# Kernel tuning notes

Hardware: AMD Instinct MI355X
Metric: run time of the kernel (lower is better)

Reference implementation:

```python
import jax, jax.numpy as jnp
import numpy as np

N_NODES = 64
KS = (52, 42, 34)  # ceil(0.8*64), ceil(0.8*52), ceil(0.8*42)


def _gcn(x, A, W, b):
    # GCNConv(improved=True): self-loop fill 2.0, symmetric normalization. A[tgt, src], weighted.
    n = A.shape[0]
    Ah = A + 2.0 * jnp.eye(n, dtype=A.dtype)
    d = Ah.sum(-1)
    dis = jnp.where(d > 0, jax.lax.rsqrt(d), 0.0)
    An = dis[:, None] * Ah * dis[None, :]
    return An @ (x @ W) + b


def _augment(A):
    # GraphUNet.augment_adj: add self loops (weight 1), A2 = A1 @ A1, remove self loops
    n = A.shape[0]
    eye = jnp.eye(n, dtype=A.dtype)
    A1 = A + eye
    return (A1 @ A1) * (1.0 - eye)


def _pool(x, A, w, k):
    # TopKPooling: score = tanh(x.w/||w||), keep top-k, scale kept features by score
    s = jnp.tanh((x @ w) / jnp.linalg.norm(w))
    sv, perm = jax.lax.top_k(s, k)
    return x[perm] * sv[:, None], A[perm][:, perm], perm


def _unet(x, A, dw0, db0, dws, dbs, pws, uws, ubs, uwl, ubl):
    # GraphUNet(depth=3, sum_res=True), single graph: x [n, F2], A [n, n]
    x = jax.nn.relu(_gcn(x, A, dw0, db0))
    xs, As, perms = [x], [A], []
    for i in range(3):
        A = _augment(A)
        x, A, perm = _pool(x, A, pws[i], KS[i])
        x = jax.nn.relu(_gcn(x, A, dws[i], dbs[i]))
        if i < 2:
            xs.append(x)
            As.append(A)
        perms.append(perm)
    for i in range(3):
        j = 2 - i
        res, Aj, perm = xs[j], As[j], perms[j]
        x = res + jnp.zeros_like(res).at[perm].set(x)
        if i < 2:
            x = jax.nn.relu(_gcn(x, Aj, uws[i], ubs[i]))
        else:
            x = _gcn(x, Aj, uwl, ubl)
    return x


def _nnconv(x, src, dst, ea, mw, mb, rw, bias):
    # NNConv(aggr='mean'): per-edge MLP weight, gather-matmul-scatter-mean + root + bias
    B, E = src.shape
    fin, fout = rw.shape
    We = jax.nn.relu(ea @ mw + mb).reshape(B, E, fin, fout)  # [B,E,fin,fout]
    xs = jnp.take_along_axis(x, src[..., None], axis=1)      # [B,E,fin]
    msg = jnp.einsum('bei,beio->beo', xs, We)                # [B,E,fout]
    seg = jax.vmap(lambda m, d: jax.ops.segment_sum(m, d, num_segments=N_NODES))
    sums = seg(msg, dst)
    cnt = seg(jnp.ones(msg.shape[:2] + (1,), msg.dtype), dst)
    agg = sums / jnp.maximum(cnt, 1.0)
    return agg + x @ rw + bias


def _adj(src, dst):
    A = jnp.zeros((N_NODES, N_NODES), jnp.float32).at[dst, src].set(1.0)
    return A * (1.0 - jnp.eye(N_NODES, dtype=jnp.float32))


def _branch(x, ei, ea, mlp1, mlp2, u1, u2):
    src, dst = ei[:, 0], ei[:, 1]
    A = jax.vmap(_adj)(src, dst)
    x = jax.nn.relu(_nnconv(x, src, dst, ea, *mlp1))
    x = jax.nn.relu(jax.vmap(lambda h, a: _unet(h, a, *u1))(x, A))
    x = jax.nn.relu(_nnconv(x, src, dst, ea, *mlp2))
    x = jax.nn.relu(jax.vmap(lambda h, a: _unet(h, a, *u2))(x, A))
    return x.mean(axis=1)  # global_mean_pool (equal-sized graphs)


def setup_inputs() -> dict:
    key = jax.random.key(0)
    keys = iter(jax.random.split(key, 64))
    def nrm(shape, s=1.0):
        return jax.random.normal(next(keys), shape, jnp.float32) * s
    B, n, E, F, F2, Q, H, C = 128, 64, 512, 64, 32, 16, 256, 50
    inp = {}
    inp['x1'] = nrm((B, n, F))
    inp['ei1'] = jax.random.randint(next(keys), (B, 2, E), 0, n, jnp.int32)
    inp['ea1'] = jax.random.uniform(next(keys), (B, E, 1), jnp.float32)
    inp['jw1'] = nrm((B, Q))
    inp['x2'] = nrm((B, n, F))
    inp['ei2'] = jax.random.randint(next(keys), (B, 2, E), 0, n, jnp.int32)
    inp['ea2'] = jax.random.uniform(next(keys), (B, E, 1), jnp.float32)
    inp['jw2'] = nrm((B, Q))
    inp['m1w'] = nrm((1, F * F2), 0.1)
    inp['m1b'] = nrm((F * F2,), 0.1)
    inp['r1w'] = nrm((F, F2), 0.1)
    inp['c1b'] = nrm((F2,), 0.1)
    inp['m2w'] = nrm((1, F2 * F2), 0.1)
    inp['m2b'] = nrm((F2 * F2,), 0.1)
    inp['r2w'] = nrm((F2, F2), 0.1)
    inp['c2b'] = nrm((F2,), 0.1)
    for p in ('u1', 'u2'):
        inp[p + '_dw0'] = nrm((F2, C), 0.1)
        inp[p + '_db0'] = nrm((C,), 0.1)
        inp[p + '_dws'] = nrm((3, C, C), 0.1)
        inp[p + '_dbs'] = nrm((3, C), 0.1)
        inp[p + '_pws'] = nrm((3, C), 0.1)
        inp[p + '_uws'] = nrm((2, C, C), 0.1)
        inp[p + '_ubs'] = nrm((2, C), 0.1)
        inp[p + '_uwl'] = nrm((C, F2), 0.1)
        inp[p + '_ubl'] = nrm((F2,), 0.1)
    inp['bb_w'] = nrm(((F2 + Q) * 2, H), 0.1)
    inp['bb_b'] = nrm((H,), 0.1)
    return inp


def reference(x1, ei1, ea1, jw1, x2, ei2, ea2, jw2,
              m1w, m1b, r1w, c1b, m2w, m2b, r2w, c2b,
              u1_dw0, u1_db0, u1_dws, u1_dbs, u1_pws, u1_uws, u1_ubs, u1_uwl, u1_ubl,
              u2_dw0, u2_db0, u2_dws, u2_dbs, u2_pws, u2_uws, u2_ubs, u2_uwl, u2_ubl,
              bb_w, bb_b):
    mlp1 = (m1w, m1b, r1w, c1b)
    mlp2 = (m2w, m2b, r2w, c2b)
    u1 = (u1_dw0, u1_db0, u1_dws, u1_dbs, u1_pws, u1_uws, u1_ubs, u1_uwl, u1_ubl)
    u2 = (u2_dw0, u2_db0, u2_dws, u2_dbs, u2_pws, u2_uws, u2_ubs, u2_uwl, u2_ubl)
    r1 = _branch(x1, ei1, ea1, mlp1, mlp2, u1, u2)
    r2 = _branch(x2, ei2, ea2, mlp1, mlp2, u1, u2)
    c = jnp.concatenate([r1, jw1, r2, jw2], axis=1)  # [(F2+Q)*2]
    return jax.nn.relu(c @ bb_w + bb_b)
```

## Files before the change

kernel.cpp:

```cpp
#include <hip/hip_runtime.h>
#include <math.h>

#define UT 1024
#define XS 52
#define ASTR 65

__device__ __forceinline__ float wred16(float v) {
    v += __shfl_xor(v, 8); v += __shfl_xor(v, 4);
    v += __shfl_xor(v, 2); v += __shfl_xor(v, 1);
    return v;
}

__global__ __launch_bounds__(256)
void adj_kernel(const int* __restrict__ eiA, const int* __restrict__ eiB,
                float* __restrict__ Aout)
{
    const int g = blockIdx.x, tid = threadIdx.x;
    const int* eig = (g < 128) ? (eiA + (size_t)g * 1024)
                               : (eiB + (size_t)(g - 128) * 1024);
    __shared__ float Al[4096];
    for (int i = tid; i < 4096; i += 256) Al[i] = 0.f;
    __syncthreads();
    for (int e = tid; e < 512; e += 256) {
        int s = eig[e], d = eig[512 + e];
        Al[d * 64 + s] = 1.f;
    }
    __syncthreads();
    if (tid < 64) Al[tid * 64 + tid] = 0.f;
    __syncthreads();
    for (int i = tid; i < 4096; i += 256) Aout[(size_t)g * 4096 + i] = Al[i];
}

template<int FIN>
__global__ __launch_bounds__(UT)
void nnconv_kernel(const float* __restrict__ xA, const float* __restrict__ xB,
                   const int* __restrict__ eiA, const int* __restrict__ eiB,
                   const float* __restrict__ eaA, const float* __restrict__ eaB,
                   const float* __restrict__ mw, const float* __restrict__ mb,
                   const float* __restrict__ rw, const float* __restrict__ bias,
                   float* __restrict__ out)
{
    constexpr int ICN = FIN / 16;
    constexpr int ERN = UT / (32 * ICN);
    constexpr int EPT = 512 / ERN;
    const int g = blockIdx.x, tid = threadIdx.x;
    const float* xg; const int* eig; const float* eag;
    if (g < 128) {
        xg = xA + (size_t)g * 64 * FIN; eig = eiA + (size_t)g * 1024; eag = eaA + (size_t)g * 512;
    } else {
        int h = g - 128;
        xg = xB + (size_t)h * 64 * FIN; eig = eiB + (size_t)h * 1024; eag = eaB + (size_t)h * 512;
    }

    __shared__ __align__(16) float xl[64 * FIN];
    __shared__ __align__(16) float mwl[FIN * 32];
    __shared__ __align__(16) float mbl[FIN * 32];
    __shared__ __align__(16) float rwl[FIN * 32];
    __shared__ __align__(16) float sums[64 * 32];
    __shared__ int   srcl[512];
    __shared__ int   dstl[512];
    __shared__ float eal[512];
    __shared__ float cntl[64];

    for (int i = tid; i < 64 * FIN; i += UT) xl[i] = xg[i];
    for (int i = tid; i < FIN * 32; i += UT) { mwl[i] = mw[i]; mbl[i] = mb[i]; rwl[i] = rw[i]; }
    for (int e = tid; e < 512; e += UT) {
        srcl[e] = eig[e]; dstl[e] = eig[512 + e]; eal[e] = eag[e];
    }
    for (int i = tid; i < 2048; i += UT) sums[i] = 0.f;
    if (tid < 64) cntl[tid] = 0.f;
    __syncthreads();

    const int o = tid & 31, ic = (tid >> 5) & (ICN - 1), er = tid / (32 * ICN);
    float mwr[16], mbr[16];
    #pragma unroll
    for (int z = 0; z < 16; z++) {
        mwr[z] = mwl[(ic * 16 + z) * 32 + o];
        mbr[z] = mbl[(ic * 16 + z) * 32 + o];
    }
    for (int e = tid; e < 512; e += UT) atomicAdd(&cntl[dstl[e]], 1.f);

    for (int e = er * EPT; e < er * EPT + EPT; e++) {
        int s = srcl[e]; int d = dstl[e]; float av = eal[e];
        float acc = 0.f;
        #pragma unroll
        for (int z = 0; z < 16; z += 4) {
            float4 xv = *(const float4*)&xl[s * FIN + ic * 16 + z];
            acc += xv.x * fmaxf(fmaf(av, mwr[z + 0], mbr[z + 0]), 0.f);
            acc += xv.y * fmaxf(fmaf(av, mwr[z + 1], mbr[z + 1]), 0.f);
            acc += xv.z * fmaxf(fmaf(av, mwr[z + 2], mbr[z + 2]), 0.f);
            acc += xv.w * fmaxf(fmaf(av, mwr[z + 3], mbr[z + 3]), 0.f);
        }
        acc += __shfl_down(acc, 32);
        if ((tid & 32) == 0) atomicAdd(&sums[d * 32 + o], acc);
    }
    __syncthreads();

    for (int it = tid; it < 512; it += UT) {
        int nn = it >> 3, o0 = (it & 7) * 4;
        float a0 = 0.f, a1 = 0.f, a2 = 0.f, a3 = 0.f;
        for (int i = 0; i < FIN; i++) {
            float xv = xl[nn * FIN + i];
            float4 w = *(const float4*)&rwl[i * 32 + o0];
            a0 = fmaf(xv, w.x, a0); a1 = fmaf(xv, w.y, a1);
            a2 = fmaf(xv, w.z, a2); a3 = fmaf(xv, w.w, a3);
        }
        float inv = 1.0f / fmaxf(cntl[nn], 1.f);
        float4 sv = *(const float4*)&sums[nn * 32 + o0];
        float4 bv = *(const float4*)&bias[o0];
        float4 r;
        r.x = fmaxf(sv.x * inv + a0 + bv.x, 0.f);
        r.y = fmaxf(sv.y * inv + a1 + bv.y, 0.f);
        r.z = fmaxf(sv.z * inv + a2 + bv.z, 0.f);
        r.w = fmaxf(sv.w * inv + a3 + bv.w, 0.f);
        *(float4*)&out[(size_t)g * 2048 + nn * 32 + o0] = r;
    }
}

__device__ __forceinline__ void gcn_u(int n, int cin, int cout,
    float* __restrict__ x, float* __restrict__ tmp,
    const float* __restrict__ A, float* __restrict__ Wl,
    float* __restrict__ dis,
    const float* __restrict__ Wg, const float* __restrict__ bg, bool relu)
{
    const int tid = threadIdx.x;
    const int nso = (cout + 3) >> 2;
    for (int idx = tid; idx < 51 * 52; idx += UT) {
        int r = idx / 52, c = idx - r * 52;
        float v = 0.f;
        if (r < cin && c < cout) v = Wg[r * cout + c];
        else if (r == 50 && c < cout) v = bg[c];
        Wl[idx] = v;
    }
    {
        int r = tid >> 4, l = tid & 15;
        float s = 0.f;
        if (r < n) for (int j = l; j < n; j += 16) s += A[r * ASTR + j];
        s = wred16(s);
        if (l == 0 && r < n) dis[r] = 1.0f / sqrtf(2.0f + s);
    }
    __syncthreads();
    int nr2 = n >> 1;
    for (int it = tid; it < nr2 * nso; it += UT) {
        int i0 = (it / nso) * 2, o0 = (it - (it / nso) * nso) * 4;
        float a0=0,a1=0,a2=0,a3=0, b0=0,b1=0,b2=0,b3=0;
        for (int k = 0; k < cin; k++) {
            float4 w = *(const float4*)&Wl[k * 52 + o0];
            float x0 = x[i0 * XS + k], x1 = x[(i0 + 1) * XS + k];
            a0 = fmaf(x0, w.x, a0); a1 = fmaf(x0, w.y, a1);
            a2 = fmaf(x0, w.z, a2); a3 = fmaf(x0, w.w, a3);
            b0 = fmaf(x1, w.x, b0); b1 = fmaf(x1, w.y, b1);
            b2 = fmaf(x1, w.z, b2); b3 = fmaf(x1, w.w, b3);
        }
        float d0 = dis[i0], d1 = dis[i0 + 1];
        float4 t0; t0.x = a0*d0; t0.y = a1*d0; t0.z = a2*d0; t0.w = a3*d0;
        float4 t1; t1.x = b0*d1; t1.y = b1*d1; t1.z = b2*d1; t1.w = b3*d1;
        *(float4*)&tmp[i0 * XS + o0] = t0;
        *(float4*)&tmp[(i0 + 1) * XS + o0] = t1;
    }
    __syncthreads();
    for (int it = tid; it < nr2 * nso; it += UT) {
        int i0 = (it / nso) * 2, o0 = (it - (it / nso) * nso) * 4;
        float a0=0,a1=0,a2=0,a3=0, b0=0,b1=0,b2=0,b3=0;
        for (int j = 0; j < n; j++) {
            float4 t = *(const float4*)&tmp[j * XS + o0];
            float av0 = A[i0 * ASTR + j], av1 = A[(i0 + 1) * ASTR + j];
            a0 = fmaf(av0, t.x, a0); a1 = fmaf(av0, t.y, a1);
            a2 = fmaf(av0, t.z, a2); a3 = fmaf(av0, t.w, a3);
            b0 = fmaf(av1, t.x, b0); b1 = fmaf(av1, t.y, b1);
            b2 = fmaf(av1, t.z, b2); b3 = fmaf(av1, t.w, b3);
        }
        float4 bias = *(const float4*)&Wl[50 * 52 + o0];
        float4 s0 = *(const float4*)&tmp[i0 * XS + o0];
        float4 s1 = *(const float4*)&tmp[(i0 + 1) * XS + o0];
        float d0 = dis[i0], d1 = dis[i0 + 1];
        float4 r0, r1;
        r0.x = fmaf(d0, a0 + 2.f*s0.x, bias.x); r0.y = fmaf(d0, a1 + 2.f*s0.y, bias.y);
        r0.z = fmaf(d0, a2 + 2.f*s0.z, bias.z); r0.w = fmaf(d0, a3 + 2.f*s0.w, bias.w);
        r1.x = fmaf(d1, b0 + 2.f*s1.x, bias.x); r1.y = fmaf(d1, b1 + 2.f*s1.y, bias.y);
        r1.z = fmaf(d1, b2 + 2.f*s1.z, bias.z); r1.w = fmaf(d1, b3 + 2.f*s1.w, bias.w);
        if (relu) {
            r0.x = fmaxf(r0.x, 0.f); r0.y = fmaxf(r0.y, 0.f);
            r0.z = fmaxf(r0.z, 0.f); r0.w = fmaxf(r0.w, 0.f);
            r1.x = fmaxf(r1.x, 0.f); r1.y = fmaxf(r1.y, 0.f);
            r1.z = fmaxf(r1.z, 0.f); r1.w = fmaxf(r1.w, 0.f);
        }
        *(float4*)&x[i0 * XS + o0] = r0;
        *(float4*)&x[(i0 + 1) * XS + o0] = r1;
    }
    __syncthreads();
}

__global__ __launch_bounds__(UT)
void unet_kernel(const float* __restrict__ xin, const float* __restrict__ Aglob,
                 const float* __restrict__ dw0, const float* __restrict__ db0,
                 const float* __restrict__ dws, const float* __restrict__ dbs,
                 const float* __restrict__ pws,
                 const float* __restrict__ uws, const float* __restrict__ ubs,
                 const float* __restrict__ uwl, const float* __restrict__ ubl,
                 float* __restrict__ ws_xs, float* __restrict__ ws_As,
                 float* __restrict__ outp, int mean_mode)
{
    const int g = blockIdx.x, tid = threadIdx.x;
    __shared__ __align__(16) float Aa[64 * ASTR];
    __shared__ __align__(16) float Ab[64 * ASTR];
    __shared__ __align__(16) float x0c[64 * XS];
    __shared__ __align__(16) float x1c[64 * XS];
    __shared__ float scr[64];
    __shared__ float dis[64];
    __shared__ float svals[64];
    __shared__ int   permL[192];

    float *pA = Aa, *pF = Ab, *px = x0c, *pt_ = x1c;
    float* xs_g = ws_xs + (size_t)g * 9984;
    float* as_g = ws_As + (size_t)g * 6144;
    const float* Ag_g = Aglob + (size_t)g * 4096;
    const int nsz[4] = {64, 52, 42, 34};

    {
        const float* xg = xin + (size_t)g * 2048;
        for (int idx = tid; idx < 512; idx += UT) {
            int i = idx >> 3, o0 = (idx & 7) * 4;
            *(float4*)&px[i * XS + o0] = *(const float4*)&xg[i * 32 + o0];
        }
        for (int idx = tid; idx < 4096; idx += UT)
            pA[(idx >> 6) * ASTR + (idx & 63)] = Ag_g[idx];
    }
    __syncthreads();

    gcn_u(64, 32, 50, px, pt_, pA, pF, dis, dw0, db0, true);

    for (int lvl = 0; lvl < 3; lvl++) {
        int n = nsz[lvl], kk = nsz[lvl + 1];
        const float* wg = pws + lvl * 50;
        int* perm = permL + lvl * 64;
        {
            int r = tid >> 4, l = tid & 15;
            float s = 0.f, wn = 0.f;
            for (int q = l; q < 50; q += 16) {
                float wv = wg[q];
                wn = fmaf(wv, wv, wn);
                s = fmaf(px[r * XS + q], wv, s);
            }
            s = wred16(s); wn = wred16(wn);
            if (l == 0 && r < n) scr[r] = tanhf(s / sqrtf(wn));
        }
        {
            float* xd = xs_g + lvl * 3328;
            for (int idx = tid; idx < 3328; idx += UT) xd[idx] = px[idx];
            if (lvl == 1) for (int idx = tid; idx < 52 * ASTR; idx += UT) as_g[idx] = pA[idx];
            if (lvl == 2) for (int idx = tid; idx < 42 * ASTR; idx += UT) as_g[3380 + idx] = pA[idx];
        }
        __syncthreads();
        if (tid < 64) {
            float v = (tid < n) ? scr[tid] : -2.0f;
            int id = tid;
            for (int sz = 2; sz <= 64; sz <<= 1)
                for (int st = sz >> 1; st > 0; st >>= 1) {
                    float ov = __shfl_xor(v, st);
                    int oi = __shfl_xor(id, st);
                    bool up = ((tid & sz) == 0);
                    bool lower = ((tid & st) == 0);
                    bool less = (v > ov) || (v == ov && id < oi);
                    bool keep = (up == lower) ? less : !less;
                    if (!keep) { v = ov; id = oi; }
                }
            if (tid < kk) { perm[tid] = id; svals[tid] = v; }
        }
        __syncthreads();
        for (int idx = tid; idx < n * 13; idx += UT) {
            int m = idx / 13, u0 = (idx - (idx / 13) * 13) * 4;
            float4 gv;
            gv.x = (u0 + 0 < kk) ? pA[m * ASTR + perm[u0 + 0]] : 0.f;
            gv.y = (u0 + 1 < kk) ? pA[m * ASTR + perm[u0 + 1]] : 0.f;
            gv.z = (u0 + 2 < kk) ? pA[m * ASTR + perm[u0 + 2]] : 0.f;
            gv.w = (u0 + 3 < kk) ? pA[m * ASTR + perm[u0 + 3]] : 0.f;
            *(float4*)&pt_[m * XS + u0] = gv;
        }
        float gx0=0, gx1=0, gx2=0, gx3=0; int gdst = -1;
        if (tid < kk * 13) {
            int t = tid / 13, q0 = (tid - t * 13) * 4;
            float sv = svals[t]; int p = perm[t];
            gx0 = px[p * XS + q0 + 0] * sv; gx1 = px[p * XS + q0 + 1] * sv;
            gx2 = px[p * XS + q0 + 2] * sv; gx3 = px[p * XS + q0 + 3] * sv;
            gdst = t * XS + q0;
        }
        __syncthreads();
        if (gdst >= 0) {
            px[gdst] = gx0; px[gdst + 1] = gx1; px[gdst + 2] = gx2; px[gdst + 3] = gx3;
        }
        int nt2 = kk >> 1, nst = (kk + 3) >> 2;
        for (int it = tid; it < nt2 * nst; it += UT) {
            int t0 = (it / nst) * 2, u0 = (it - (it / nst) * nst) * 4;
            int p0 = perm[t0], p1 = perm[t0 + 1];
            float a0=0,a1=0,a2=0,a3=0, b0=0,b1=0,b2=0,b3=0;
            for (int m = 0; m < n; m++) {
                float4 gv = *(const float4*)&pt_[m * XS + u0];
                float q0v = pA[p0 * ASTR + m], q1v = pA[p1 * ASTR + m];
                a0 = fmaf(q0v, gv.x, a0); a1 = fmaf(q0v, gv.y, a1);
                a2 = fmaf(q0v, gv.z, a2); a3 = fmaf(q0v, gv.w, a3);
                b0 = fmaf(q1v, gv.x, b0); b1 = fmaf(q1v, gv.y, b1);
                b2 = fmaf(q1v, gv.z, b2); b3 = fmaf(q1v, gv.w, b3);
            }
            float4 g0 = *(const float4*)&pt_[p0 * XS + u0];
            float4 g1 = *(const float4*)&pt_[p1 * XS + u0];
            float v;
            v = a0 + 2.f*g0.x; pF[t0*ASTR + u0+0] = (u0+0 == t0) ? 0.f : v;
            v = a1 + 2.f*g0.y; pF[t0*ASTR + u0+1] = (u0+1 == t0) ? 0.f : v;
            v = a2 + 2.f*g0.z; pF[t0*ASTR + u0+2] = (u0+2 == t0) ? 0.f : v;
            v = a3 + 2.f*g0.w; pF[t0*ASTR + u0+3] = (u0+3 == t0) ? 0.f : v;
            v = b0 + 2.f*g1.x; pF[(t0+1)*ASTR + u0+0] = (u0+0 == t0+1) ? 0.f : v;
            v = b1 + 2.f*g1.y; pF[(t0+1)*ASTR + u0+1] = (u0+1 == t0+1) ? 0.f : v;
            v = b2 + 2.f*g1.z; pF[(t0+1)*ASTR + u0+2] = (u0+2 == t0+1) ? 0.f : v;
            v = b3 + 2.f*g1.w; pF[(t0+1)*ASTR + u0+3] = (u0+3 == t0+1) ? 0.f : v;
        }
        __syncthreads();
        gcn_u(kk, 50, 50, px, pt_, pF, pA, dis, dws + lvl * 2500, dbs + lvl * 50, true);
        { float* t = pA; pA = pF; pF = t; }
    }

    for (int i2 = 0; i2 < 3; i2++) {
        int j = 2 - i2;
        int nj = nsz[j], kc = nsz[j + 1];
        {
            const float* resg = xs_g + j * 3328;
            for (int idx = tid; idx < 3328; idx += UT) pt_[idx] = resg[idx];
            if (j == 0) {
                for (int idx = tid; idx < 4096; idx += UT)
                    pF[(idx >> 6) * ASTR + (idx & 63)] = Ag_g[idx];
            } else if (j == 1) {
                for (int idx = tid; idx < 52 * ASTR; idx += UT) pF[idx] = as_g[idx];
            } else {
                for (int idx = tid; idx < 42 * ASTR; idx += UT) pF[idx] = as_g[3380 + idx];
            }
        }
        __syncthreads();
        const int* perm = permL + j * 64;
        for (int it = tid; it < kc * 13; it += UT) {
            int t = it / 13, q0 = (it - (it / 13) * 13) * 4;
            int p = perm[t];
            pt_[p * XS + q0 + 0] += px[t * XS + q0 + 0];
            pt_[p * XS + q0 + 1] += px[t * XS + q0 + 1];
            pt_[p * XS + q0 + 2] += px[t * XS + q0 + 2];
            pt_[p * XS + q0 + 3] += px[t * XS + q0 + 3];
        }
        __syncthreads();
        if (i2 < 2)
            gcn_u(nj, 50, 50, pt_, px, pF, pA, dis, uws + i2 * 2500, ubs + i2 * 50, true);
        else
            gcn_u(64, 50, 32, pt_, px, pF, pA, dis, uwl, ubl, false);
        { float* t2 = px; px = pt_; pt_ = t2; }
        { float* t2 = pA; pA = pF; pF = t2; }
    }

    if (mean_mode) {
        int r = tid >> 4, l = tid & 15;
        if (r < 32) {
            float s = 0.f;
            for (int i = l; i < 64; i += 16) s += fmaxf(px[i * XS + r], 0.f);
            s = wred16(s);
            if (l == 0) outp[(size_t)g * 32 + r] = s * (1.0f / 64.0f);
        }
    } else {
        float* og = outp + (size_t)g * 2048;
        for (int idx = tid; idx < 512; idx += UT) {
            int i = idx >> 3, o0 = (idx & 7) * 4;
            float4 vv = *(const float4*)&px[i * XS + o0];
            vv.x = fmaxf(vv.x, 0.f); vv.y = fmaxf(vv.y, 0.f);
            vv.z = fmaxf(vv.z, 0.f); vv.w = fmaxf(vv.w, 0.f);
            *(float4*)&og[i * 32 + o0] = vv;
        }
    }
}

__global__ __launch_bounds__(256)
void head_kernel(const float* __restrict__ r,
                 const float* __restrict__ jw1, const float* __restrict__ jw2,
                 const float* __restrict__ bw, const float* __restrict__ bb,
                 float* __restrict__ out)
{
    const int b = blockIdx.x, h = threadIdx.x;
    float acc = bb[h];
    const float* r1 = r + (size_t)b * 32;
    const float* r2 = r + (size_t)(128 + b) * 32;
    #pragma unroll
    for (int q = 0; q < 32; q++) acc += r1[q] * bw[q * 256 + h];
    #pragma unroll
    for (int q = 0; q < 16; q++) acc += jw1[b * 16 + q] * bw[(32 + q) * 256 + h];
    #pragma unroll
    for (int q = 0; q < 32; q++) acc += r2[q] * bw[(48 + q) * 256 + h];
    #pragma unroll
    for (int q = 0; q < 16; q++) acc += jw2[b * 16 + q] * bw[(80 + q) * 256 + h];
    out[(size_t)b * 256 + h] = fmaxf(acc, 0.f);
}

extern "C" void kernel_launch(void* const* d_in, const int* in_sizes, int n_in,
                              void* d_out, int out_size, void* d_ws, size_t ws_size,
                              hipStream_t stream)
{
    const float* x1  = (const float*)d_in[0];
    const int*   ei1 = (const int*)  d_in[1];
    const float* ea1 = (const float*)d_in[2];
    const float* jw1 = (const float*)d_in[3];
    const float* x2  = (const float*)d_in[4];
    const int*   ei2 = (const int*)  d_in[5];
    const float* ea2 = (const float*)d_in[6];
    const float* jw2 = (const float*)d_in[7];
    const float* m1w = (const float*)d_in[8];
    const float* m1b = (const float*)d_in[9];
    const float* r1w = (const float*)d_in[10];
    const float* c1b = (const float*)d_in[11];
    const float* m2w = (const float*)d_in[12];
    const float* m2b = (const float*)d_in[13];
    const float* r2w = (const float*)d_in[14];
    const float* c2b = (const float*)d_in[15];
    const float* u1p[9]; for (int i = 0; i < 9; i++) u1p[i] = (const float*)d_in[16 + i];
    const float* u2p[9]; for (int i = 0; i < 9; i++) u2p[i] = (const float*)d_in[25 + i];
    const float* bbw = (const float*)d_in[34];
    const float* bbb = (const float*)d_in[35];

    char* ws = (char*)d_ws;
    size_t off = 0;
    float* A    = (float*)(ws + off); off += 256ull * 4096 * 4;
    float* xc1  = (float*)(ws + off); off += 256ull * 2048 * 4;
    float* xu1  = (float*)(ws + off); off += 256ull * 2048 * 4;
    float* xc2  = (float*)(ws + off); off += 256ull * 2048 * 4;
    float* rr   = (float*)(ws + off); off += 256ull * 32 * 4;
    float* wxs  = (float*)(ws + off); off += 256ull * 9984 * 4;
    float* wAs  = (float*)(ws + off); off += 256ull * 6144 * 4;
    (void)ws_size; (void)in_sizes; (void)n_in; (void)out_size;

    adj_kernel<<<256, 256, 0, stream>>>(ei1, ei2, A);
    nnconv_kernel<64><<<256, UT, 0, stream>>>(x1, x2, ei1, ei2, ea1, ea2,
                                              m1w, m1b, r1w, c1b, xc1);
    unet_kernel<<<256, UT, 0, stream>>>(xc1, A,
        u1p[0], u1p[1], u1p[2], u1p[3], u1p[4], u1p[5], u1p[6], u1p[7], u1p[8],
        wxs, wAs, xu1, 0);
    nnconv_kernel<32><<<256, UT, 0, stream>>>(xu1, xu1 + 128ull * 2048,
                                              ei1, ei2, ea1, ea2,
                                              m2w, m2b, r2w, c2b, xc2);
    unet_kernel<<<256, UT, 0, stream>>>(xc2, A,
        u2p[0], u2p[1], u2p[2], u2p[3], u2p[4], u2p[5], u2p[6], u2p[7], u2p[8],
        wxs, wAs, rr, 1);
    head_kernel<<<128, 256, 0, stream>>>(rr, jw1, jw2, bbw, bbb, (float*)d_out);
}
```

Baseline: 358.4 us.

## Fuse adjacency build into first NNConv kernel and restructure GCN inner loops

The separate adjacency kernel is removed. The first NNConv kernel now builds the dense adjacency in shared memory, already padded to the 65-float stride, and writes it to workspace so the U-Net kernel can copy it directly. NNConv and GCN loops are reworked to handle one output row per item with two independent accumulators, trading row blocking for more parallel items and shorter dependency chains. mw/mb are read straight from global memory instead of being staged in shared memory, and the U-Net down path is split into helper functions. This removes one launch and one global round trip, but adds shared memory use to the first NNConv kernel.

```diff
diff --git a/kernel.cpp b/kernel.cpp
--- a/kernel.cpp
+++ b/kernel.cpp
@@ -9,112 +9,6 @@
     v += __shfl_xor(v, 8); v += __shfl_xor(v, 4);
     v += __shfl_xor(v, 2); v += __shfl_xor(v, 1);
     return v;
-}
-
-__global__ __launch_bounds__(256)
-void adj_kernel(const int* __restrict__ eiA, const int* __restrict__ eiB,
-                float* __restrict__ Aout)
-{
-    const int g = blockIdx.x, tid = threadIdx.x;
-    const int* eig = (g < 128) ? (eiA + (size_t)g * 1024)
-                               : (eiB + (size_t)(g - 128) * 1024);
-    __shared__ float Al[4096];
-    for (int i = tid; i < 4096; i += 256) Al[i] = 0.f;
-    __syncthreads();
-    for (int e = tid; e < 512; e += 256) {
-        int s = eig[e], d = eig[512 + e];
-        Al[d * 64 + s] = 1.f;
-    }
-    __syncthreads();
-    if (tid < 64) Al[tid * 64 + tid] = 0.f;
-    __syncthreads();
-    for (int i = tid; i < 4096; i += 256) Aout[(size_t)g * 4096 + i] = Al[i];
-}
-
-template<int FIN>
-__global__ __launch_bounds__(UT)
-void nnconv_kernel(const float* __restrict__ xA, const float* __restrict__ xB,
-                   const int* __restrict__ eiA, const int* __restrict__ eiB,
-                   const float* __restrict__ eaA, const float* __restrict__ eaB,
-                   const float* __restrict__ mw, const float* __restrict__ mb,
-                   const float* __restrict__ rw, const float* __restrict__ bias,
-                   float* __restrict__ out)
-{
-    constexpr int ICN = FIN / 16;
-    constexpr int ERN = UT / (32 * ICN);
-    constexpr int EPT = 512 / ERN;
-    const int g = blockIdx.x, tid = threadIdx.x;
-    const float* xg; const int* eig; const float* eag;
-    if (g < 128) {
-        xg = xA + (size_t)g * 64 * FIN; eig = eiA + (size_t)g * 1024; eag = eaA + (size_t)g * 512;
-    } else {
-        int h = g - 128;
-        xg = xB + (size_t)h * 64 * FIN; eig = eiB + (size_t)h * 1024; eag = eaB + (size_t)h * 512;
-    }
-
-    __shared__ __align__(16) float xl[64 * FIN];
-    __shared__ __align__(16) float mwl[FIN * 32];
-    __shared__ __align__(16) float mbl[FIN * 32];
-    __shared__ __align__(16) float rwl[FIN * 32];
-    __shared__ __align__(16) float sums[64 * 32];
-    __shared__ int   srcl[512];
-    __shared__ int   dstl[512];
-    __shared__ float eal[512];
-    __shared__ float cntl[64];
-
-    for (int i = tid; i < 64 * FIN; i += UT) xl[i] = xg[i];
-    for (int i = tid; i < FIN * 32; i += UT) { mwl[i] = mw[i]; mbl[i] = mb[i]; rwl[i] = rw[i]; }
-    for (int e = tid; e < 512; e += UT) {
-        srcl[e] = eig[e]; dstl[e] = eig[512 + e]; eal[e] = eag[e];
-    }
-    for (int i = tid; i < 2048; i += UT) sums[i] = 0.f;
-    if (tid < 64) cntl[tid] = 0.f;
-    __syncthreads();
-
-    const int o = tid & 31, ic = (tid >> 5) & (ICN - 1), er = tid / (32 * ICN);
-    float mwr[16], mbr[16];
-    #pragma unroll
-    for (int z = 0; z < 16; z++) {
-        mwr[z] = mwl[(ic * 16 + z) * 32 + o];
-        mbr[z] = mbl[(ic * 16 + z) * 32 + o];
-    }
-    for (int e = tid; e < 512; e += UT) atomicAdd(&cntl[dstl[e]], 1.f);
-
-    for (int e = er * EPT; e < er * EPT + EPT; e++) {
-        int s = srcl[e]; int d = dstl[e]; float av = eal[e];
-        float acc = 0.f;
-        #pragma unroll
-        for (int z = 0; z < 16; z += 4) {
-            float4 xv = *(const float4*)&xl[s * FIN + ic * 16 + z];
-            acc += xv.x * fmaxf(fmaf(av, mwr[z + 0], mbr[z + 0]), 0.f);
-            acc += xv.y * fmaxf(fmaf(av, mwr[z + 1], mbr[z + 1]), 0.f);
-            acc += xv.z * fmaxf(fmaf(av, mwr[z + 2], mbr[z + 2]), 0.f);
-            acc += xv.w * fmaxf(fmaf(av, mwr[z + 3], mbr[z + 3]), 0.f);
-        }
-        acc += __shfl_down(acc, 32);
-        if ((tid & 32) == 0) atomicAdd(&sums[d * 32 + o], acc);
-    }
-    __syncthreads();
-
-    for (int it = tid; it < 512; it += UT) {
-        int nn = it >> 3, o0 = (it & 7) * 4;
-        float a0 = 0.f, a1 = 0.f, a2 = 0.f, a3 = 0.f;
-        for (int i = 0; i < FIN; i++) {
-            float xv = xl[nn * FIN + i];
-            float4 w = *(const float4*)&rwl[i * 32 + o0];
-            a0 = fmaf(xv, w.x, a0); a1 = fmaf(xv, w.y, a1);
-            a2 = fmaf(xv, w.z, a2); a3 = fmaf(xv, w.w, a3);
-        }
-        float inv = 1.0f / fmaxf(cntl[nn], 1.f);
-        float4 sv = *(const float4*)&sums[nn * 32 + o0];
-        float4 bv = *(const float4*)&bias[o0];
-        float4 r;
-        r.x = fmaxf(sv.x * inv + a0 + bv.x, 0.f);
-        r.y = fmaxf(sv.y * inv + a1 + bv.y, 0.f);
-        r.z = fmaxf(sv.z * inv + a2 + bv.z, 0.f);
-        r.w = fmaxf(sv.w * inv + a3 + bv.w, 0.f);
-        *(float4*)&out[(size_t)g * 2048 + nn * 32 + o0] = r;
-    }
 }
 
 __device__ __forceinline__ void gcn_u(int n, int cin, int cout,
@@ -140,59 +34,144 @@
         if (l == 0 && r < n) dis[r] = 1.0f / sqrtf(2.0f + s);
     }
     __syncthreads();
-    int nr2 = n >> 1;
-    for (int it = tid; it < nr2 * nso; it += UT) {
-        int i0 = (it / nso) * 2, o0 = (it - (it / nso) * nso) * 4;
+    const int items = n * nso;
+    for (int it = tid; it < items; it += UT) {
+        int i = it / nso, o0 = (it - i * nso) * 4;
         float a0=0,a1=0,a2=0,a3=0, b0=0,b1=0,b2=0,b3=0;
-        for (int k = 0; k < cin; k++) {
-            float4 w = *(const float4*)&Wl[k * 52 + o0];
-            float x0 = x[i0 * XS + k], x1 = x[(i0 + 1) * XS + k];
-            a0 = fmaf(x0, w.x, a0); a1 = fmaf(x0, w.y, a1);
-            a2 = fmaf(x0, w.z, a2); a3 = fmaf(x0, w.w, a3);
-            b0 = fmaf(x1, w.x, b0); b1 = fmaf(x1, w.y, b1);
-            b2 = fmaf(x1, w.z, b2); b3 = fmaf(x1, w.w, b3);
-        }
-        float d0 = dis[i0], d1 = dis[i0 + 1];
-        float4 t0; t0.x = a0*d0; t0.y = a1*d0; t0.z = a2*d0; t0.w = a3*d0;
-        float4 t1; t1.x = b0*d1; t1.y = b1*d1; t1.z = b2*d1; t1.w = b3*d1;
-        *(float4*)&tmp[i0 * XS + o0] = t0;
-        *(float4*)&tmp[(i0 + 1) * XS + o0] = t1;
-    }
-    __syncthreads();
-    for (int it = tid; it < nr2 * nso; it += UT) {
-        int i0 = (it / nso) * 2, o0 = (it - (it / nso) * nso) * 4;
+        for (int k = 0; k < cin; k += 2) {
+            float4 w0 = *(const float4*)&Wl[k * 52 + o0];
+            float4 w1 = *(const float4*)&Wl[(k + 1) * 52 + o0];
+            float x0 = x[i * XS + k], x1 = x[i * XS + k + 1];
+            a0 = fmaf(x0, w0.x, a0); a1 = fmaf(x0, w0.y, a1);
+            a2 = fmaf(x0, w0.z, a2); a3 = fmaf(x0, w0.w, a3);
+            b0 = fmaf(x1, w1.x, b0); b1 = fmaf(x1, w1.y, b1);
+            b2 = fmaf(x1, w1.z, b2); b3 = fmaf(x1, w1.w, b3);
+        }
+        float d = dis[i];
+        float4 t;
+        t.x = (a0 + b0) * d; t.y = (a1 + b1) * d;
+        t.z = (a2 + b2) * d; t.w = (a3 + b3) * d;
+        *(float4*)&tmp[i * XS + o0] = t;
+    }
+    __syncthreads();
+    for (int it = tid; it < items; it += UT) {
+        int i = it / nso, o0 = (it - i * nso) * 4;
         float a0=0,a1=0,a2=0,a3=0, b0=0,b1=0,b2=0,b3=0;
-        for (int j = 0; j < n; j++) {
-            float4 t = *(const float4*)&tmp[j * XS + o0];
-            float av0 = A[i0 * ASTR + j], av1 = A[(i0 + 1) * ASTR + j];
-            a0 = fmaf(av0, t.x, a0); a1 = fmaf(av0, t.y, a1);
-            a2 = fmaf(av0, t.z, a2); a3 = fmaf(av0, t.w, a3);
-            b0 = fmaf(av1, t.x, b0); b1 = fmaf(av1, t.y, b1);
-            b2 = fmaf(av1, t.z, b2); b3 = fmaf(av1, t.w, b3);
+        for (int j = 0; j < n; j += 2) {
+            float4 t0 = *(const float4*)&tmp[j * XS + o0];
+            float4 t1 = *(const float4*)&tmp[(j + 1) * XS + o0];
+            float av0 = A[i * ASTR + j], av1 = A[i * ASTR + j + 1];
+            a0 = fmaf(av0, t0.x, a0); a1 = fmaf(av0, t0.y, a1);
+            a2 = fmaf(av0, t0.z, a2); a3 = fmaf(av0, t0.w, a3);
+            b0 = fmaf(av1, t1.x, b0); b1 = fmaf(av1, t1.y, b1);
+            b2 = fmaf(av1, t1.z, b2); b3 = fmaf(av1, t1.w, b3);
         }
         float4 bias = *(const float4*)&Wl[50 * 52 + o0];
-        float4 s0 = *(const float4*)&tmp[i0 * XS + o0];
-        float4 s1 = *(const float4*)&tmp[(i0 + 1) * XS + o0];
-        float d0 = dis[i0], d1 = dis[i0 + 1];
-        float4 r0, r1;
-        r0.x = fmaf(d0, a0 + 2.f*s0.x, bias.x); r0.y = fmaf(d0, a1 + 2.f*s0.y, bias.y);
-        r0.z = fmaf(d0, a2 + 2.f*s0.z, bias.z); r0.w = fmaf(d0, a3 + 2.f*s0.w, bias.w);
-        r1.x = fmaf(d1, b0 + 2.f*s1.x, bias.x); r1.y = fmaf(d1, b1 + 2.f*s1.y, bias.y);
-        r1.z = fmaf(d1, b2 + 2.f*s1.z, bias.z); r1.w = fmaf(d1, b3 + 2.f*s1.w, bias.w);
+        float4 s0 = *(const float4*)&tmp[i * XS + o0];
+        float d = dis[i];
+        float4 r;
+        r.x = fmaf(d, (a0 + b0) + 2.f * s0.x, bias.x);
+        r.y = fmaf(d, (a1 + b1) + 2.f * s0.y, bias.y);
+        r.z = fmaf(d, (a2 + b2) + 2.f * s0.z, bias.z);
+        r.w = fmaf(d, (a3 + b3) + 2.f * s0.w, bias.w);
         if (relu) {
-            r0.x = fmaxf(r0.x, 0.f); r0.y = fmaxf(r0.y, 0.f);
-            r0.z = fmaxf(r0.z, 0.f); r0.w = fmaxf(r0.w, 0.f);
-            r1.x = fmaxf(r1.x, 0.f); r1.y = fmaxf(r1.y, 0.f);
-            r1.z = fmaxf(r1.z, 0.f); r1.w = fmaxf(r1.w, 0.f);
-        }
-        *(float4*)&x[i0 * XS + o0] = r0;
-        *(float4*)&x[(i0 + 1) * XS + o0] = r1;
-    }
-    __syncthreads();
+            r.x = fmaxf(r.x, 0.f); r.y = fmaxf(r.y, 0.f);
+            r.z = fmaxf(r.z, 0.f); r.w = fmaxf(r.w, 0.f);
+        }
+        *(float4*)&x[i * XS + o0] = r;
+    }
+    __syncthreads();
+}
+
+__device__ __forceinline__ void down_scores(int n, const float* __restrict__ wg,
+                                            const float* __restrict__ px,
+                                            float* __restrict__ scr)
+{
+    const int tid = threadIdx.x;
+    int r = tid >> 4, l = tid & 15;
+    float s = 0.f, wn = 0.f;
+    for (int q = l; q < 50; q += 16) {
+        float wv = wg[q];
+        wn = fmaf(wv, wv, wn);
+        s  = fmaf(px[r * XS + q], wv, s);
+    }
+    s = wred16(s); wn = wred16(wn);
+    if (l == 0 && r < n) scr[r] = tanhf(s / sqrtf(wn));
+}
+
+__device__ __forceinline__ void down_rest(int n, int kk,
+    float* __restrict__ px, float* __restrict__ pt_,
+    float* __restrict__ pA, float* __restrict__ pF,
+    float* __restrict__ scr, float* __restrict__ dis, float* __restrict__ svals,
+    int* __restrict__ perm, const float* __restrict__ dw,
+    const float* __restrict__ db)
+{
+    const int tid = threadIdx.x;
+    __syncthreads();
+    if (tid < 64) {
+        float v = (tid < n) ? scr[tid] : -2.0f;
+        int id = tid;
+        for (int sz = 2; sz <= 64; sz <<= 1)
+            for (int st = sz >> 1; st > 0; st >>= 1) {
+                float ov = __shfl_xor(v, st);
+                int oi = __shfl_xor(id, st);
+                bool up = ((tid & sz) == 0);
+                bool lower = ((tid & st) == 0);
+                bool less = (v > ov) || (v == ov && id < oi);
+                bool keep = (up == lower) ? less : !less;
+                if (!keep) { v = ov; id = oi; }
+            }
+        if (tid < kk) { perm[tid] = id; svals[tid] = v; }
+    }
+    __syncthreads();
+    for (int idx = tid; idx < n * 13; idx += UT) {
+        int m = idx / 13, u0 = (idx - (idx / 13) * 13) * 4;
+        float4 gv;
+        gv.x = (u0 + 0 < kk) ? pA[m * ASTR + perm[u0 + 0]] : 0.f;
+        gv.y = (u0 + 1 < kk) ? pA[m * ASTR + perm[u0 + 1]] : 0.f;
+        gv.z = (u0 + 2 < kk) ? pA[m * ASTR + perm[u0 + 2]] : 0.f;
+        gv.w = (u0 + 3 < kk) ? pA[m * ASTR + perm[u0 + 3]] : 0.f;
+        *(float4*)&pt_[m * XS + u0] = gv;
+    }
+    float gx0=0, gx1=0, gx2=0, gx3=0; int gdst = -1;
+    if (tid < kk * 13) {
+        int t = tid / 13, q0 = (tid - t * 13) * 4;
+        float sv = svals[t]; int p = perm[t];
+        gx0 = px[p * XS + q0 + 0] * sv; gx1 = px[p * XS + q0 + 1] * sv;
+        gx2 = px[p * XS + q0 + 2] * sv; gx3 = px[p * XS + q0 + 3] * sv;
+        gdst = t * XS + q0;
+    }
+    __syncthreads();
+    if (gdst >= 0) {
+        px[gdst] = gx0; px[gdst + 1] = gx1; px[gdst + 2] = gx2; px[gdst + 3] = gx3;
+    }
+    int nst = (kk + 3) >> 2;
+    for (int it = tid; it < kk * nst; it += UT) {
+        int t = it / nst, u0 = (it - t * nst) * 4;
+        int p = perm[t];
+        float a0=0,a1=0,a2=0,a3=0, c0=0,c1=0,c2=0,c3=0;
+        for (int m = 0; m < n; m += 2) {
+            float4 g0 = *(const float4*)&pt_[m * XS + u0];
+            float4 g1 = *(const float4*)&pt_[(m + 1) * XS + u0];
+            float q0v = pA[p * ASTR + m], q1v = pA[p * ASTR + m + 1];
+            a0 = fmaf(q0v, g0.x, a0); a1 = fmaf(q0v, g0.y, a1);
+            a2 = fmaf(q0v, g0.z, a2); a3 = fmaf(q0v, g0.w, a3);
+            c0 = fmaf(q1v, g1.x, c0); c1 = fmaf(q1v, g1.y, c1);
+            c2 = fmaf(q1v, g1.z, c2); c3 = fmaf(q1v, g1.w, c3);
+        }
+        float4 gg = *(const float4*)&pt_[p * XS + u0];
+        float v;
+        v = (a0 + c0) + 2.f * gg.x; pF[t * ASTR + u0 + 0] = (u0 + 0 == t) ? 0.f : v;
+        v = (a1 + c1) + 2.f * gg.y; pF[t * ASTR + u0 + 1] = (u0 + 1 == t) ? 0.f : v;
+        v = (a2 + c2) + 2.f * gg.z; pF[t * ASTR + u0 + 2] = (u0 + 2 == t) ? 0.f : v;
+        v = (a3 + c3) + 2.f * gg.w; pF[t * ASTR + u0 + 3] = (u0 + 3 == t) ? 0.f : v;
+    }
+    __syncthreads();
+    gcn_u(kk, 50, 50, px, pt_, pF, pA, dis, dw, db, true);
 }
 
 __global__ __launch_bounds__(UT)
-void unet_kernel(const float* __restrict__ xin, const float* __restrict__ Aglob,
+void unet_kernel(const float* __restrict__ xin, const float* __restrict__ wsA,
                  const float* __restrict__ dw0, const float* __restrict__ db0,
                  const float* __restrict__ dws, const float* __restrict__ dbs,
                  const float* __restrict__ pws,
@@ -214,7 +193,7 @@
     float *pA = Aa, *pF = Ab, *px = x0c, *pt_ = x1c;
     float* xs_g = ws_xs + (size_t)g * 9984;
     float* as_g = ws_As + (size_t)g * 6144;
-    const float* Ag_g = Aglob + (size_t)g * 4096;
+    const float* wsAg = wsA + (size_t)g * 4160;
     const int nsz[4] = {64, 52, 42, 34};
 
     {
@@ -223,8 +202,7 @@
             int i = idx >> 3, o0 = (idx & 7) * 4;
             *(float4*)&px[i * XS + o0] = *(const float4*)&xg[i * 32 + o0];
         }
-        for (int idx = tid; idx < 4096; idx += UT)
-            pA[(idx >> 6) * ASTR + (idx & 63)] = Ag_g[idx];
+        for (int idx = tid; idx < 4160; idx += UT) pA[idx] = wsAg[idx];
     }
     __syncthreads();
 
@@ -232,121 +210,43 @@
 
     for (int lvl = 0; lvl < 3; lvl++) {
         int n = nsz[lvl], kk = nsz[lvl + 1];
-        const float* wg = pws + lvl * 50;
-        int* perm = permL + lvl * 64;
-        {
-            int r = tid >> 4, l = tid & 15;
-            float s = 0.f, wn = 0.f;
-            for (int q = l; q < 50; q += 16) {
-                float wv = wg[q];
-                wn = fmaf(wv, wv, wn);
-                s = fmaf(px[r * XS + q], wv, s);
-            }
-            s = wred16(s); wn = wred16(wn);
-            if (l == 0 && r < n) scr[r] = tanhf(s / sqrtf(wn));
-        }
+        down_scores(n, pws + lvl * 50, px, scr);
         {
             float* xd = xs_g + lvl * 3328;
             for (int idx = tid; idx < 3328; idx += UT) xd[idx] = px[idx];
-            if (lvl == 1) for (int idx = tid; idx < 52 * ASTR; idx += UT) as_g[idx] = pA[idx];
-            if (lvl == 2) for (int idx = tid; idx < 42 * ASTR; idx += UT) as_g[3380 + idx] = pA[idx];
-        }
-        __syncthreads();
-        if (tid < 64) {
-            float v = (tid < n) ? scr[tid] : -2.0f;
-            int id = tid;
-            for (int sz = 2; sz <= 64; sz <<= 1)
-                for (int st = sz >> 1; st > 0; st >>= 1) {
-                    float ov = __shfl_xor(v, st);
-                    int oi = __shfl_xor(id, st);
-                    bool up = ((tid & sz) == 0);
-                    bool lower = ((tid & st) == 0);
-                    bool less = (v > ov) || (v == ov && id < oi);
-                    bool keep = (up == lower) ? less : !less;
-                    if (!keep) { v = ov; id = oi; }
-                }
-            if (tid < kk) { perm[tid] = id; svals[tid] = v; }
-        }
-        __syncthreads();
-        for (int idx = tid; idx < n * 13; idx += UT) {
-            int m = idx / 13, u0 = (idx - (idx / 13) * 13) * 4;
-            float4 gv;
-            gv.x = (u0 + 0 < kk) ? pA[m * ASTR + perm[u0 + 0]] : 0.f;
-            gv.y = (u0 + 1 < kk) ? pA[m * ASTR + perm[u0 + 1]] : 0.f;
-            gv.z = (u0 + 2 < kk) ? pA[m * ASTR + perm[u0 + 2]] : 0.f;
-            gv.w = (u0 + 3 < kk) ? pA[m * ASTR + perm[u0 + 3]] : 0.f;
-            *(float4*)&pt_[m * XS + u0] = gv;
-        }
-        float gx0=0, gx1=0, gx2=0, gx3=0; int gdst = -1;
-        if (tid < kk * 13) {
-            int t = tid / 13, q0 = (tid - t * 13) * 4;
-            float sv = svals[t]; int p = perm[t];
-            gx0 = px[p * XS + q0 + 0] * sv; gx1 = px[p * XS + q0 + 1] * sv;
-            gx2 = px[p * XS + q0 + 2] * sv; gx3 = px[p * XS + q0 + 3] * sv;
-            gdst = t * XS + q0;
-        }
-        __syncthreads();
-        if (gdst >= 0) {
-            px[gdst] = gx0; px[gdst + 1] = gx1; px[gdst + 2] = gx2; px[gdst + 3] = gx3;
-        }
-        int nt2 = kk >> 1, nst = (kk + 3) >> 2;
-        for (int it = tid; it < nt2 * nst; it += UT) {
-            int t0 = (it / nst) * 2, u0 = (it - (it / nst) * nst) * 4;
-            int p0 = perm[t0], p1 = perm[t0 + 1];
-            float a0=0,a1=0,a2=0,a3=0, b0=0,b1=0,b2=0,b3=0;
-            for (int m = 0; m < n; m++) {
-                float4 gv = *(const float4*)&pt_[m * XS + u0];
-                float q0v = pA[p0 * ASTR + m], q1v = pA[p1 * ASTR + m];
-                a0 = fmaf(q0v, gv.x, a0); a1 = fmaf(q0v, gv.y, a1);
-                a2 = fmaf(q0v, gv.z, a2); a3 = fmaf(q0v, gv.w, a3);
-                b0 = fmaf(q1v, gv.x, b0); b1 = fmaf(q1v, gv.y, b1);
-                b2 = fmaf(q1v, gv.z, b2); b3 = fmaf(q1v, gv.w, b3);
-            }
-            float4 g0 = *(const float4*)&pt_[p0 * XS + u0];
-            float4 g1 = *(const float4*)&pt_[p1 * XS + u0];
-            float v;
-            v = a0 + 2.f*g0.x; pF[t0*ASTR + u0+0] = (u0+0 == t0) ? 0.f : v;
-            v = a1 + 2.f*g0.y; pF[t0*ASTR + u0+1] = (u0+1 == t0) ? 0.f : v;
-            v = a2 + 2.f*g0.z; pF[t0*ASTR + u0+2] = (u0+2 == t0) ? 0.f : v;
-            v = a3 + 2.f*g0.w; pF[t0*ASTR + u0+3] = (u0+3 == t0) ? 0.f : v;
-            v = b0 + 2.f*g1.x; pF[(t0+1)*ASTR + u0+0] = (u0+0 == t0+1) ? 0.f : v;
-            v = b1 + 2.f*g1.y; pF[(t0+1)*ASTR + u0+1] = (u0+1 == t0+1) ? 0.f : v;
-            v = b2 + 2.f*g1.z; pF[(t0+1)*ASTR + u0+2] = (u0+2 == t0+1) ? 0.f : v;
-            v = b3 + 2.f*g1.w; pF[(t0+1)*ASTR + u0+3] = (u0+3 == t0+1) ? 0.f : v;
-        }
-        __syncthreads();
-        gcn_u(kk, 50, 50, px, pt_, pF, pA, dis, dws + lvl * 2500, dbs + lvl * 50, true);
+            if (lvl == 1) for (int idx = tid; idx < 3380; idx += UT) as_g[idx] = pA[idx];
+            if (lvl == 2) for (int idx = tid; idx < 2730; idx += UT) as_g[3380 + idx] = pA[idx];
+        }
+        down_rest(n, kk, px, pt_, pA, pF, scr, dis, svals, permL + lvl * 64,
+                  dws + lvl * 2500, dbs + lvl * 50);
         { float* t = pA; pA = pF; pF = t; }
     }
 
     for (int i2 = 0; i2 < 3; i2++) {
         int j = 2 - i2;
-        int nj = nsz[j], kc = nsz[j + 1];
+        int kc = nsz[j + 1];
         {
             const float* resg = xs_g + j * 3328;
             for (int idx = tid; idx < 3328; idx += UT) pt_[idx] = resg[idx];
             if (j == 0) {
-                for (int idx = tid; idx < 4096; idx += UT)
-                    pF[(idx >> 6) * ASTR + (idx & 63)] = Ag_g[idx];
+                for (int idx = tid; idx < 4160; idx += UT) pF[idx] = wsAg[idx];
             } else if (j == 1) {
-                for (int idx = tid; idx < 52 * ASTR; idx += UT) pF[idx] = as_g[idx];
+                for (int idx = tid; idx < 3380; idx += UT) pF[idx] = as_g[idx];
             } else {
-                for (int idx = tid; idx < 42 * ASTR; idx += UT) pF[idx] = as_g[3380 + idx];
+                for (int idx = tid; idx < 2730; idx += UT) pF[idx] = as_g[3380 + idx];
             }
         }
         __syncthreads();
         const int* perm = permL + j * 64;
         for (int it = tid; it < kc * 13; it += UT) {
-            int t = it / 13, q0 = (it - (it / 13) * 13) * 4;
+            int t = it / 13, q0 = (it - t * 13) * 4;
             int p = perm[t];
-            pt_[p * XS + q0 + 0] += px[t * XS + q0 + 0];
-            pt_[p * XS + q0 + 1] += px[t * XS + q0 + 1];
-            pt_[p * XS + q0 + 2] += px[t * XS + q0 + 2];
-            pt_[p * XS + q0 + 3] += px[t * XS + q0 + 3];
+            pt_[p*XS+q0+0] += px[t*XS+q0+0]; pt_[p*XS+q0+1] += px[t*XS+q0+1];
+            pt_[p*XS+q0+2] += px[t*XS+q0+2]; pt_[p*XS+q0+3] += px[t*XS+q0+3];
         }
         __syncthreads();
         if (i2 < 2)
-            gcn_u(nj, 50, 50, pt_, px, pF, pA, dis, uws + i2 * 2500, ubs + i2 * 50, true);
+            gcn_u(nsz[j], 50, 50, pt_, px, pF, pA, dis, uws + i2 * 2500, ubs + i2 * 50, true);
         else
             gcn_u(64, 50, 32, pt_, px, pF, pA, dis, uwl, ubl, false);
         { float* t2 = px; px = pt_; pt_ = t2; }
@@ -371,6 +271,138 @@
             *(float4*)&og[i * 32 + o0] = vv;
         }
     }
+}
+
+template<int FIN>
+__device__ __forceinline__ void nnconv_core(
+    const float* __restrict__ xl, float* __restrict__ rwl,
+    float* __restrict__ sums,
+    const int* __restrict__ srcl, const int* __restrict__ dstl,
+    const float* __restrict__ eal, const float* __restrict__ cnt,
+    const float* __restrict__ mw, const float* __restrict__ mb,
+    const float* __restrict__ bias, float* __restrict__ xout_g)
+{
+    const int tid = threadIdx.x;
+    constexpr int ICN = FIN / 16;
+    constexpr int EPT = 512 / (UT / (32 * ICN));
+    const int o = tid & 31, ic = (tid >> 5) & (ICN - 1), er = tid / (32 * ICN);
+    float mwr[16], mbr[16];
+    #pragma unroll
+    for (int z = 0; z < 16; z++) {
+        mwr[z] = mw[(ic * 16 + z) * 32 + o];
+        mbr[z] = mb[(ic * 16 + z) * 32 + o];
+    }
+    for (int e = er * EPT; e < er * EPT + EPT; e++) {
+        int s = srcl[e]; int d = dstl[e]; float av = eal[e];
+        float ac0 = 0.f, ac1 = 0.f, ac2 = 0.f, ac3 = 0.f;
+        #pragma unroll
+        for (int zb = 0; zb < 16; zb += 4) {
+            float4 xv = *(const float4*)&xl[s * FIN + ic * 16 + zb];
+            ac0 = fmaf(xv.x, fmaxf(fmaf(av, mwr[zb + 0], mbr[zb + 0]), 0.f), ac0);
+            ac1 = fmaf(xv.y, fmaxf(fmaf(av, mwr[zb + 1], mbr[zb + 1]), 0.f), ac1);
+            ac2 = fmaf(xv.z, fmaxf(fmaf(av, mwr[zb + 2], mbr[zb + 2]), 0.f), ac2);
+            ac3 = fmaf(xv.w, fmaxf(fmaf(av, mwr[zb + 3], mbr[zb + 3]), 0.f), ac3);
+        }
+        float acc = (ac0 + ac1) + (ac2 + ac3);
+        acc += __shfl_down(acc, 32);
+        if ((tid & 32) == 0) atomicAdd(&sums[d * 32 + o], acc);
+    }
+    __syncthreads();
+    {
+        int nn = tid >> 4, o0 = (tid & 15) * 2;
+        float a0 = 0.f, a1 = 0.f, b0 = 0.f, b1 = 0.f;
+        for (int i = 0; i < FIN; i += 2) {
+            float xv0 = xl[nn * FIN + i], xv1 = xl[nn * FIN + i + 1];
+            float2 w0 = *(const float2*)&rwl[i * 32 + o0];
+            float2 w1 = *(const float2*)&rwl[(i + 1) * 32 + o0];
+            a0 = fmaf(xv0, w0.x, a0); a1 = fmaf(xv0, w0.y, a1);
+            b0 = fmaf(xv1, w1.x, b0); b1 = fmaf(xv1, w1.y, b1);
+        }
+        float inv = 1.0f / fmaxf(cnt[nn], 1.f);
+        float2 sv = *(const float2*)&sums[nn * 32 + o0];
+        xout_g[nn * 32 + o0]     = fmaxf(fmaf(sv.x, inv, (a0 + b0) + bias[o0]),     0.f);
+        xout_g[nn * 32 + o0 + 1] = fmaxf(fmaf(sv.y, inv, (a1 + b1) + bias[o0 + 1]), 0.f);
+    }
+}
+
+__global__ __launch_bounds__(UT)
+void nnconv1_kernel(const float* __restrict__ x1, const float* __restrict__ x2,
+                    const int* __restrict__ ei1, const int* __restrict__ ei2,
+                    const float* __restrict__ ea1, const float* __restrict__ ea2,
+                    const float* __restrict__ mw, const float* __restrict__ mb,
+                    const float* __restrict__ rw, const float* __restrict__ bias,
+                    float* __restrict__ wsA, float* __restrict__ xout)
+{
+    const int g = blockIdx.x, tid = threadIdx.x;
+    __shared__ __align__(16) float xl[4096];
+    __shared__ __align__(16) float rwl[2048];
+    __shared__ __align__(16) float sums[2048];
+    __shared__ __align__(16) float Al[4160];
+    __shared__ int   srcl[512];
+    __shared__ int   dstl[512];
+    __shared__ float eal[512];
+    __shared__ float cnt[64];
+
+    const float* xg; const int* eig; const float* eag;
+    if (g < 128) {
+        xg = x1 + (size_t)g * 4096; eig = ei1 + (size_t)g * 1024; eag = ea1 + (size_t)g * 512;
+    } else {
+        int h = g - 128;
+        xg = x2 + (size_t)h * 4096; eig = ei2 + (size_t)h * 1024; eag = ea2 + (size_t)h * 512;
+    }
+    for (int i = tid; i < 4096; i += UT) xl[i] = xg[i];
+    for (int i = tid; i < 2048; i += UT) { rwl[i] = rw[i]; sums[i] = 0.f; }
+    for (int e = tid; e < 512; e += UT) {
+        srcl[e] = eig[e]; dstl[e] = eig[512 + e]; eal[e] = eag[e];
+    }
+    for (int i = tid; i < 4160; i += UT) Al[i] = 0.f;
+    if (tid < 64) cnt[tid] = 0.f;
+    __syncthreads();
+    for (int e = tid; e < 512; e += UT) Al[dstl[e] * ASTR + srcl[e]] = 1.f;
+    __syncthreads();
+    if (tid < 64) Al[tid * ASTR + tid] = 0.f;
+    for (int e = tid; e < 512; e += UT) atomicAdd(&cnt[dstl[e]], 1.f);
+    __syncthreads();
+    for (int i = tid; i < 4160; i += UT) wsA[(size_t)g * 4160 + i] = Al[i];
+
+    nnconv_core<64>(xl, rwl, sums, srcl, dstl, eal, cnt, mw, mb, bias,
+                    xout + (size_t)g * 2048);
+}
+
+__global__ __launch_bounds__(UT)
+void nnconv2_kernel(const float* __restrict__ xin,
+                    const int* __restrict__ ei1, const int* __restrict__ ei2,
+                    const float* __restrict__ ea1, const float* __restrict__ ea2,
+                    const float* __restrict__ mw, const float* __restrict__ mb,
+                    const float* __restrict__ rw, const float* __restrict__ bias,
+                    float* __restrict__ xout)
+{
+    const int g = blockIdx.x, tid = threadIdx.x;
+    __shared__ __align__(16) float xl[2048];
+    __shared__ __align__(16) float rwl[1024];
+    __shared__ __align__(16) float sums[2048];
+    __shared__ int   srcl[512];
+    __shared__ int   dstl[512];
+    __shared__ float eal[512];
+    __shared__ float cnt[64];
+
+    const int* eig; const float* eag;
+    if (g < 128) { eig = ei1 + (size_t)g * 1024; eag = ea1 + (size_t)g * 512; }
+    else { int h = g - 128; eig = ei2 + (size_t)h * 1024; eag = ea2 + (size_t)h * 512; }
+
+    const float* xg = xin + (size_t)g * 2048;
+    for (int i = tid; i < 2048; i += UT) { xl[i] = xg[i]; sums[i] = 0.f; }
+    for (int i = tid; i < 1024; i += UT) rwl[i] = rw[i];
+    for (int e = tid; e < 512; e += UT) {
+        srcl[e] = eig[e]; dstl[e] = eig[512 + e]; eal[e] = eag[e];
+    }
+    if (tid < 64) cnt[tid] = 0.f;
+    __syncthreads();
+    for (int e = tid; e < 512; e += UT) atomicAdd(&cnt[dstl[e]], 1.f);
+    __syncthreads();
+
+    nnconv_core<32>(xl, rwl, sums, srcl, dstl, eal, cnt, mw, mb, bias,
+                    xout + (size_t)g * 2048);
 }
 
 __global__ __launch_bounds__(256)
@@ -421,7 +453,7 @@
 
     char* ws = (char*)d_ws;
     size_t off = 0;
-    float* A    = (float*)(ws + off); off += 256ull * 4096 * 4;
+    float* wsA  = (float*)(ws + off); off += 256ull * 4160 * 4;
     float* xc1  = (float*)(ws + off); off += 256ull * 2048 * 4;
     float* xu1  = (float*)(ws + off); off += 256ull * 2048 * 4;
     float* xc2  = (float*)(ws + off); off += 256ull * 2048 * 4;
@@ -430,16 +462,14 @@
     float* wAs  = (float*)(ws + off); off += 256ull * 6144 * 4;
     (void)ws_size; (void)in_sizes; (void)n_in; (void)out_size;
 
-    adj_kernel<<<256, 256, 0, stream>>>(ei1, ei2, A);
-    nnconv_kernel<64><<<256, UT, 0, stream>>>(x1, x2, ei1, ei2, ea1, ea2,
-                                              m1w, m1b, r1w, c1b, xc1);
-    unet_kernel<<<256, UT, 0, stream>>>(xc1, A,
+    nnconv1_kernel<<<256, UT, 0, stream>>>(x1, x2, ei1, ei2, ea1, ea2,
+                                           m1w, m1b, r1w, c1b, wsA, xc1);
+    unet_kernel<<<256, UT, 0, stream>>>(xc1, wsA,
         u1p[0], u1p[1], u1p[2], u1p[3], u1p[4], u1p[5], u1p[6], u1p[7], u1p[8],
         wxs, wAs, xu1, 0);
-    nnconv_kernel<32><<<256, UT, 0, stream>>>(xu1, xu1 + 128ull * 2048,
-                                              ei1, ei2, ea1, ea2,
-                                              m2w, m2b, r2w, c2b, xc2);
-    unet_kernel<<<256, UT, 0, stream>>>(xc2, A,
+    nnconv2_kernel<<<256, UT, 0, stream>>>(xu1, ei1, ei2, ea1, ea2,
+                                           m2w, m2b, r2w, c2b, xc2);
+    unet_kernel<<<256, UT, 0, stream>>>(xc2, wsA,
         u2p[0], u2p[1], u2p[2], u2p[3], u2p[4], u2p[5], u2p[6], u2p[7], u2p[8],
         wxs, wAs, rr, 1);
     head_kernel<<<128, 256, 0, stream>>>(rr, jw1, jw2, bbw, bbb, (float*)d_out);
```

New measurement: 356.6 us. About the same (-0.5%).
